# Optimization experiments

Hardware: AMD Instinct MI355X
Metric: run time of the kernel (lower is better)

## Reference

```python
import jax, jax.numpy as jnp
import numpy as np

B, T, D, H = 256, 512, 128, 256


def setup_inputs() -> dict:
    key = jax.random.key(0)
    ks = jax.random.split(key, 8)
    return {
        "x": jax.random.normal(ks[0], (B, T, D), jnp.float32),
        "m": jax.random.randint(ks[1], (B, T, D), 0, 2, jnp.int32),
        "s": jax.random.uniform(ks[2], (B, T, 1), jnp.float32),
        "kernel": jax.random.normal(ks[3], (D, 3 * H), jnp.float32) * 0.05,
        "recurrent_kernel": jax.random.normal(ks[4], (H, 3 * H), jnp.float32) * 0.05,
        "masking_kernel": jax.random.normal(ks[5], (D, 3 * H), jnp.float32) * 0.05,
        "bias": jnp.zeros((3 * H,), jnp.float32),
        "input_decay_kernel": jax.random.normal(ks[6], (D,), jnp.float32) * 0.05,
        "input_decay_bias": jnp.zeros((D,), jnp.float32),
        "hidden_decay_kernel": jax.random.normal(ks[7], (D, H), jnp.float32) * 0.05,
        "hidden_decay_bias": jnp.zeros((H,), jnp.float32),
    }


def _grud_scan(x, m, s, kernel, recurrent_kernel, masking_kernel, bias,
               input_decay_kernel, input_decay_bias,
               hidden_decay_kernel, hidden_decay_bias):
    b, t, d = x.shape
    h = recurrent_kernel.shape[0]
    mf = m.astype(x.dtype)
    mb = m > 0  # boolean mask, K.switch semantics
    # mask projection is h-independent -> hoist the big GEMM out of the scan
    mproj = jnp.einsum('btd,dk->btk', mf, masking_kernel)  # [B,T,3H]
    Kz, Kr, Kh = kernel[:, :h], kernel[:, h:2 * h], kernel[:, 2 * h:]
    Rz, Rr, Rh = recurrent_kernel[:, :h], recurrent_kernel[:, h:2 * h], recurrent_kernel[:, 2 * h:]
    bz, br, bh = bias[:h], bias[h:2 * h], bias[2 * h:]

    def step(carry, inp):
        h_tm1, x_keep, s_prev = carry
        xt, mbt, st, mpt = inp  # xt [B,D], mbt [B,D] bool, st [B,1], mpt [B,3H]
        d_t = st - s_prev  # [B,D] via broadcast
        gamma_di = jnp.exp(-jax.nn.relu(d_t * input_decay_kernel + input_decay_bias))
        gamma_dh = jnp.exp(-jax.nn.relu(d_t @ hidden_decay_kernel + hidden_decay_bias))
        x_keep_t = jnp.where(mbt, xt, x_keep)
        x_t = jnp.where(mbt, xt, gamma_di * x_keep_t)
        h_d = gamma_dh * h_tm1
        mz, mr, mh = mpt[:, :h], mpt[:, h:2 * h], mpt[:, 2 * h:]
        z_t = jax.nn.sigmoid(x_t @ Kz + h_d @ Rz + mz + bz)
        r_pre = x_t @ Kr + h_d @ Rr + mr + br  # original uses pre-activation r in hh
        hh_t = jnp.tanh(x_t @ Kh + (r_pre * h_d) @ Rh + mh + bh)
        h_t = z_t * h_tm1 + (1.0 - z_t) * hh_t
        s_keep = jnp.where(mbt, jnp.broadcast_to(st, s_prev.shape), s_prev)
        return (h_t, x_keep_t, s_keep), h_t

    init = (jnp.zeros((b, h), x.dtype), jnp.zeros((b, d), x.dtype), jnp.zeros((b, d), x.dtype))
    xs = (jnp.swapaxes(x, 0, 1), jnp.swapaxes(mb, 0, 1),
          jnp.swapaxes(s, 0, 1), jnp.swapaxes(mproj, 0, 1))
    _, hs = jax.lax.scan(step, init, xs)  # hs: [T,B,H]
    return jnp.swapaxes(hs, 0, 1)  # [B,T,H]


def reference(x, m, s, kernel, recurrent_kernel, masking_kernel, bias,
              input_decay_kernel, input_decay_bias,
              hidden_decay_kernel, hidden_decay_bias):
    return _grud_scan(x, m, s, kernel, recurrent_kernel, masking_kernel, bias,
                      input_decay_kernel, input_decay_bias,
                      hidden_decay_kernel, hidden_decay_bias)
```

## Files before the change

kernel.cpp:

```cpp
#include <hip/hip_runtime.h>
#include <hip/hip_bf16.h>
#include <cstdint>


#define Bsz 256
#define Tsz 512
#define Dsz 128
#define Hsz 256
#define BT  (Bsz * Tsz)
#define N3H 768

typedef __attribute__((ext_vector_type(8))) short   short8;
typedef __attribute__((ext_vector_type(8))) __bf16  bf16x8;
typedef __attribute__((ext_vector_type(4))) float   f32x4;

__device__ __forceinline__ unsigned short f2bf(float f) {
    union { float f; unsigned u; } v; v.f = f;
    unsigned r = v.u + 0x7fffu + ((v.u >> 16) & 1u);
    return (unsigned short)(r >> 16);
}
__device__ __forceinline__ float b2f(unsigned short u) {
    union { unsigned u; float f; } v; v.u = ((unsigned)u) << 16;
    return v.f;
}
__device__ __forceinline__ bf16x8 ld_frag(const unsigned short* p) {
    short8 v = *(const short8*)p;
    return __builtin_bit_cast(bf16x8, v);
}

__device__ __forceinline__ void barrier_lds() {
    asm volatile("s_waitcnt lgkmcnt(0)\n\ts_barrier" ::: "memory");
}

__global__ void k_pack(const float* __restrict__ kern, const float* __restrict__ maskk,
                       const float* __restrict__ rk,   const float* __restrict__ hdk,
                       unsigned short* __restrict__ KM_T, unsigned short* __restrict__ R_T,
                       unsigned short* __restrict__ W_T) {
    int i = blockIdx.x * 256 + threadIdx.x;
    if (i < N3H * 256) {
        int n = i >> 8, k = i & 255;
        float v = (k < 128) ? kern[k * N3H + n] : maskk[(k - 128) * N3H + n];
        KM_T[i] = f2bf(v);
        R_T[i]  = f2bf(rk[k * N3H + n]);
    } else {
        int j = i - N3H * 256;
        if (j < 256 * 128) {
            int n = j >> 7, k = j & 127;
            W_T[j] = f2bf(hdk[k * 256 + n]);
        }
    }
}

__global__ __launch_bounds__(256) void k_locf(
        const float* __restrict__ x, const int* __restrict__ m,
        const float* __restrict__ s, const float* __restrict__ wdi,
        const float* __restrict__ bdi,
        unsigned short* __restrict__ X2, unsigned short* __restrict__ Dt) {
    int gid = blockIdx.x * blockDim.x + threadIdx.x;
    int b = gid >> 7, d = gid & 127;
    float w  = wdi[d], bi = bdi[d];
    float x_keep = 0.f, s_prev = 0.f;
    const float* xb  = x + (size_t)b * Tsz * Dsz + d;
    const int*   mb_ = m + (size_t)b * Tsz * Dsz + d;
    const float* sb  = s + (size_t)b * Tsz;
    unsigned short* X2b = X2 + (size_t)b * Tsz * 256 + d;
    unsigned short* Dtb = Dt + (size_t)b * Tsz * 128 + d;
    for (int t0 = 0; t0 < Tsz; t0 += 4) {
        float xv[4], sv[4]; int mv[4];
#pragma unroll
        for (int u = 0; u < 4; u++) {
            xv[u] = xb[(size_t)(t0 + u) * Dsz];
            mv[u] = mb_[(size_t)(t0 + u) * Dsz];
            sv[u] = sb[t0 + u];
        }
#pragma unroll
        for (int u = 0; u < 4; u++) {
            int t = t0 + u;
            float dt  = sv[u] - s_prev;
            float gdi = __expf(-fmaxf(dt * w + bi, 0.f));
            bool  mbt = mv[u] > 0;
            if (mbt) x_keep = xv[u];
            float xe = mbt ? xv[u] : gdi * x_keep;
            if (mbt) s_prev = sv[u];
            X2b[(size_t)t * 256]       = f2bf(xe);
            X2b[(size_t)t * 256 + 128] = f2bf((float)mv[u]);
            Dtb[(size_t)t * 128]       = f2bf(dt);
        }
    }
}

template <int MODE, int K, int N>
__global__ __launch_bounds__(256) void k_gemm(
        const unsigned short* __restrict__ A, const unsigned short* __restrict__ Bt,
        const float* __restrict__ bias, unsigned short* __restrict__ C) {
    __shared__ unsigned short As[128][40];
    __shared__ unsigned short Bs[128][40];
    int m0 = blockIdx.x * 128, n0 = blockIdx.y * 128;
    int tid = threadIdx.x, lane = tid & 63, w = tid >> 6;
    int wm = w & 1, wn = w >> 1;
    int r15 = lane & 15, q = lane >> 4;
    int arow = tid >> 2, akg = tid & 3;
    f32x4 acc[4][4];
#pragma unroll
    for (int i = 0; i < 4; i++)
#pragma unroll
        for (int j = 0; j < 4; j++) acc[i][j] = f32x4{0.f, 0.f, 0.f, 0.f};

    for (int kk = 0; kk < K; kk += 32) {
        short8 av0 = *(const short8*)(A  + (size_t)(m0 + arow)      * K + kk + akg * 8);
        short8 av1 = *(const short8*)(A  + (size_t)(m0 + arow + 64) * K + kk + akg * 8);
        short8 bv0 = *(const short8*)(Bt + (size_t)(n0 + arow)      * K + kk + akg * 8);
        short8 bv1 = *(const short8*)(Bt + (size_t)(n0 + arow + 64) * K + kk + akg * 8);
        *(short8*)&As[arow][akg * 8]      = av0;
        *(short8*)&As[arow + 64][akg * 8] = av1;
        *(short8*)&Bs[arow][akg * 8]      = bv0;
        *(short8*)&Bs[arow + 64][akg * 8] = bv1;
        __syncthreads();
        bf16x8 af[4], bf[4];
#pragma unroll
        for (int i = 0; i < 4; i++) af[i] = ld_frag(&As[wm * 64 + i * 16 + r15][q * 8]);
#pragma unroll
        for (int j = 0; j < 4; j++) bf[j] = ld_frag(&Bs[wn * 64 + j * 16 + r15][q * 8]);
#pragma unroll
        for (int i = 0; i < 4; i++)
#pragma unroll
            for (int j = 0; j < 4; j++)
                acc[i][j] = __builtin_amdgcn_mfma_f32_16x16x32_bf16(af[i], bf[j], acc[i][j], 0, 0, 0);
        __syncthreads();
    }
#pragma unroll
    for (int i = 0; i < 4; i++)
#pragma unroll
        for (int j = 0; j < 4; j++) {
            int col = n0 + wn * 64 + j * 16 + r15;
            float bs = bias[col];
#pragma unroll
            for (int rg = 0; rg < 4; rg++) {
                int row = m0 + wm * 64 + i * 16 + q * 4 + rg;
                float v = acc[i][j][rg] + bs;
                if (MODE == 1) v = __expf(-fmaxf(v, 0.f));
                C[(size_t)row * N + col] = f2bf(v);
            }
        }
}

__global__ __launch_bounds__(512, 2) void k_scan(
        const unsigned short* __restrict__ Apre, const unsigned short* __restrict__ G,
        const unsigned short* __restrict__ R_T, float* __restrict__ out) {
    int b = blockIdx.x;
    int tid = threadIdx.x, lane = tid & 63, w = tid >> 6;
    int r15 = lane & 15, q = lane >> 4;

    __shared__ __align__(16) unsigned short hd_bf[256];
    __shared__ __align__(16) unsigned short u_bf[256];
    __shared__ __align__(16) unsigned short ap_l[2][768];
    __shared__ __align__(16) unsigned short g_l[2][256];

    bf16x8 fzr[4][8];
    bf16x8 fh[2][8];
#pragma unroll
    for (int nt = 0; nt < 4; nt++) {
        int col = (nt < 2) ? (w * 32 + nt * 16 + r15)
                           : (256 + w * 32 + (nt - 2) * 16 + r15);
        const unsigned short* base = R_T + (size_t)col * 256 + q * 8;
#pragma unroll
        for (int kt = 0; kt < 8; kt++) {
            fzr[nt][kt] = ld_frag(base + kt * 32);
            asm volatile("" : "+v"(fzr[nt][kt]));
        }
    }
#pragma unroll
    for (int nt = 0; nt < 2; nt++) {
        const unsigned short* base = R_T + (size_t)(512 + w * 32 + nt * 16 + r15) * 256 + q * 8;
#pragma unroll
        for (int kt = 0; kt < 8; kt++) {
            fh[nt][kt] = ld_frag(base + kt * 32);
            asm volatile("" : "+v"(fh[nt][kt]));
        }
    }

    if (tid < 256) hd_bf[tid] = 0;

    const unsigned short* aprow = Apre + (size_t)b * Tsz * N3H;
    const unsigned short* grow  = G    + (size_t)b * Tsz * 256;

    if (tid < 192)      *(uint2*)&ap_l[0][tid * 4]         = *(const uint2*)(aprow + tid * 4);
    else if (tid < 384) *(uint2*)&ap_l[1][(tid-192) * 4]   = *(const uint2*)(aprow + N3H + (tid-192) * 4);
    else if (tid < 448) *(uint2*)&g_l[0][(tid-384) * 4]    = *(const uint2*)(grow + (tid-384) * 4);
    else                *(uint2*)&g_l[1][(tid-448) * 4]    = *(const uint2*)(grow + 256 + (tid-448) * 4);
    __syncthreads();

    bool hiSel  = (q >= 2);
    bool writer = ((q & 1) == 0);
    int  col    = w * 32 + (hiSel ? 16 : 0) + r15;
    float h_reg  = 0.f;
    float hd_reg = 0.f;

    float* outb = out + (size_t)b * Tsz * 256;
    for (int t = 0; t < Tsz; t++) {
        int buf = t & 1;
        int tp2 = (t + 2 < Tsz) ? t + 2 : Tsz - 1;
        unsigned pf;
        if (tid < 384) pf = *(const unsigned*)(aprow + (size_t)tp2 * N3H + tid * 2);
        else           pf = *(const unsigned*)(grow  + (size_t)tp2 * 256 + (tid - 384) * 2);

        unsigned short a_z = ap_l[buf][col];
        unsigned short a_r = ap_l[buf][256 + col];
        unsigned short a_h = ap_l[buf][512 + col];

        f32x4 acc[4];
#pragma unroll
        for (int nt = 0; nt < 4; nt++) acc[nt] = f32x4{0.f, 0.f, 0.f, 0.f};
#pragma unroll
        for (int kt = 0; kt < 8; kt++) {
            bf16x8 afr = ld_frag(&hd_bf[kt * 32 + q * 8]);
#pragma unroll
            for (int nt = 0; nt < 4; nt++)
                acc[nt] = __builtin_amdgcn_mfma_f32_16x16x32_bf16(afr, fzr[nt][kt], acc[nt], 0, 0, 0);
        }
        float pz = (hiSel ? acc[1][0] : acc[0][0]) + b2f(a_z);
        float pr = (hiSel ? acc[3][0] : acc[2][0]) + b2f(a_r);
        float u  = pr * hd_reg;
        if (writer) u_bf[col] = f2bf(u);
        barrier_lds();

        unsigned short g_v = g_l[buf ^ 1][col];
        f32x4 acch[2];
#pragma unroll
        for (int nt = 0; nt < 2; nt++) acch[nt] = f32x4{0.f, 0.f, 0.f, 0.f};
#pragma unroll
        for (int kt = 0; kt < 8; kt++) {
            bf16x8 afr = ld_frag(&u_bf[kt * 32 + q * 8]);
#pragma unroll
            for (int nt = 0; nt < 2; nt++)
                acch[nt] = __builtin_amdgcn_mfma_f32_16x16x32_bf16(afr, fh[nt][kt], acch[nt], 0, 0, 0);
        }
        float z = 1.f / (1.f + __expf(-pz));
        float ph = (hiSel ? acch[1][0] : acch[0][0]) + b2f(a_h);
        float e2 = __expf(2.f * ph);
        float hh = 1.f - 2.f / (e2 + 1.f);
        float hn = z * h_reg + (1.f - z) * hh;
        h_reg = hn;
        if (writer) outb[(size_t)t * 256 + col] = hn;
        hd_reg = b2f(g_v) * hn;
        if (writer) hd_bf[col] = f2bf(hd_reg);
        barrier_lds();

        if (tid < 384) *(unsigned*)&ap_l[buf][tid * 2] = pf;
        else           *(unsigned*)&g_l[buf][(tid - 384) * 2] = pf;
    }
}

extern "C" void kernel_launch(void* const* d_in, const int* in_sizes, int n_in,
                              void* d_out, int out_size, void* d_ws, size_t ws_size,
                              hipStream_t stream) {
    const float* x    = (const float*)d_in[0];
    const int*   m    = (const int*)  d_in[1];
    const float* s    = (const float*)d_in[2];
    const float* kern = (const float*)d_in[3];
    const float* rk   = (const float*)d_in[4];
    const float* mk   = (const float*)d_in[5];
    const float* bias = (const float*)d_in[6];
    const float* wdi  = (const float*)d_in[7];
    const float* bdi  = (const float*)d_in[8];
    const float* hdk  = (const float*)d_in[9];
    const float* hdb  = (const float*)d_in[10];
    float* out = (float*)d_out;

    char* ws = (char*)d_ws;
    size_t off = 0;
    auto alloc = [&](size_t bytes) -> void* {
        void* p = ws + off; off += (bytes + 255) & ~(size_t)255; return p;
    };
    unsigned short* X2   = (unsigned short*)alloc((size_t)BT * 256 * 2);
    unsigned short* Dt   = (unsigned short*)alloc((size_t)BT * 128 * 2);
    unsigned short* Apre = (unsigned short*)alloc((size_t)BT * N3H * 2);
    unsigned short* Gm   = (unsigned short*)alloc((size_t)BT * 256 * 2);
    unsigned short* KM_T = (unsigned short*)alloc((size_t)N3H * 256 * 2);
    unsigned short* R_T  = (unsigned short*)alloc((size_t)N3H * 256 * 2);
    unsigned short* W_T  = (unsigned short*)alloc((size_t)256 * 128 * 2);
    (void)ws_size; (void)in_sizes; (void)n_in; (void)out_size;

    k_pack<<<dim3((N3H * 256 + 256 * 128 + 255) / 256), dim3(256), 0, stream>>>(
        kern, mk, rk, hdk, KM_T, R_T, W_T);
    k_locf<<<dim3(Bsz * Dsz / 256), dim3(256), 0, stream>>>(x, m, s, wdi, bdi, X2, Dt);
    k_gemm<0, 256, N3H><<<dim3(BT / 128, N3H / 128), dim3(256), 0, stream>>>(X2, KM_T, bias, Apre);
    k_gemm<1, 128, 256><<<dim3(BT / 128, 256 / 128), dim3(256), 0, stream>>>(Dt, W_T, hdb, Gm);
    k_scan<<<dim3(Bsz), dim3(512), 0, stream>>>(Apre, Gm, R_T, out);
}
```

Before: 1.066 ms.

## Load GEMM tiles straight into LDS with XOR swizzle and swap grid order

Result: no change. 1.071 ms (+0.4%).

```diff
diff --git a/kernel.cpp b/kernel.cpp
--- a/kernel.cpp
+++ b/kernel.cpp
@@ -13,6 +13,9 @@
 typedef __attribute__((ext_vector_type(8))) short   short8;
 typedef __attribute__((ext_vector_type(8))) __bf16  bf16x8;
 typedef __attribute__((ext_vector_type(4))) float   f32x4;
+
+typedef const __attribute__((address_space(1))) unsigned char gas_t;
+typedef __attribute__((address_space(3))) unsigned char las_t;
 
 __device__ __forceinline__ unsigned short f2bf(float f) {
     union { float f; unsigned u; } v; v.f = f;
@@ -93,13 +96,15 @@
 __global__ __launch_bounds__(256) void k_gemm(
         const unsigned short* __restrict__ A, const unsigned short* __restrict__ Bt,
         const float* __restrict__ bias, unsigned short* __restrict__ C) {
-    __shared__ unsigned short As[128][40];
-    __shared__ unsigned short Bs[128][40];
-    int m0 = blockIdx.x * 128, n0 = blockIdx.y * 128;
+    __shared__ unsigned short As[128 * 32];
+    __shared__ unsigned short Bs[128 * 32];
+    int n0 = blockIdx.x * 128, m0 = blockIdx.y * 128;
     int tid = threadIdx.x, lane = tid & 63, w = tid >> 6;
     int wm = w & 1, wn = w >> 1;
     int r15 = lane & 15, q = lane >> 4;
-    int arow = tid >> 2, akg = tid & 3;
+
+    int srow0 = w * 16 + (lane >> 2);
+    int chnkL = lane & 3;
     f32x4 acc[4][4];
 #pragma unroll
     for (int i = 0; i < 4; i++)
@@ -107,20 +112,29 @@
         for (int j = 0; j < 4; j++) acc[i][j] = f32x4{0.f, 0.f, 0.f, 0.f};
 
     for (int kk = 0; kk < K; kk += 32) {
-        short8 av0 = *(const short8*)(A  + (size_t)(m0 + arow)      * K + kk + akg * 8);
-        short8 av1 = *(const short8*)(A  + (size_t)(m0 + arow + 64) * K + kk + akg * 8);
-        short8 bv0 = *(const short8*)(Bt + (size_t)(n0 + arow)      * K + kk + akg * 8);
-        short8 bv1 = *(const short8*)(Bt + (size_t)(n0 + arow + 64) * K + kk + akg * 8);
-        *(short8*)&As[arow][akg * 8]      = av0;
-        *(short8*)&As[arow + 64][akg * 8] = av1;
-        *(short8*)&Bs[arow][akg * 8]      = bv0;
-        *(short8*)&Bs[arow + 64][akg * 8] = bv1;
+#pragma unroll
+        for (int j = 0; j < 2; j++) {
+            int row = srow0 + j * 64;
+            int csrc = chnkL ^ (row & 3);
+            const unsigned short* ga = A  + (size_t)(m0 + row) * K + kk + csrc * 8;
+            const unsigned short* gb = Bt + (size_t)(n0 + row) * K + kk + csrc * 8;
+            las_t* la = (las_t*)As + (size_t)(j * 4096 + w * 1024 + (lane & 63) * 16);
+            las_t* lb = (las_t*)Bs + (size_t)(j * 4096 + w * 1024 + (lane & 63) * 16);
+            __builtin_amdgcn_global_load_lds((gas_t*)ga, la, 16, 0, 0);
+            __builtin_amdgcn_global_load_lds((gas_t*)gb, lb, 16, 0, 0);
+        }
         __syncthreads();
         bf16x8 af[4], bf[4];
 #pragma unroll
-        for (int i = 0; i < 4; i++) af[i] = ld_frag(&As[wm * 64 + i * 16 + r15][q * 8]);
-#pragma unroll
-        for (int j = 0; j < 4; j++) bf[j] = ld_frag(&Bs[wn * 64 + j * 16 + r15][q * 8]);
+        for (int i = 0; i < 4; i++) {
+            int row = wm * 64 + i * 16 + r15;
+            af[i] = ld_frag(&As[row * 32 + ((q ^ (row & 3)) << 3)]);
+        }
+#pragma unroll
+        for (int j = 0; j < 4; j++) {
+            int row = wn * 64 + j * 16 + r15;
+            bf[j] = ld_frag(&Bs[row * 32 + ((q ^ (row & 3)) << 3)]);
+        }
 #pragma unroll
         for (int i = 0; i < 4; i++)
 #pragma unroll
@@ -226,14 +240,13 @@
 
         unsigned short g_v = g_l[buf ^ 1][col];
         f32x4 acch[2];
-#pragma unroll
-        for (int nt = 0; nt < 2; nt++) acch[nt] = f32x4{0.f, 0.f, 0.f, 0.f};
+        acch[0] = f32x4{0.f, 0.f, 0.f, 0.f};
+        acch[1] = f32x4{0.f, 0.f, 0.f, 0.f};
 #pragma unroll
         for (int kt = 0; kt < 8; kt++) {
             bf16x8 afr = ld_frag(&u_bf[kt * 32 + q * 8]);
-#pragma unroll
-            for (int nt = 0; nt < 2; nt++)
-                acch[nt] = __builtin_amdgcn_mfma_f32_16x16x32_bf16(afr, fh[nt][kt], acch[nt], 0, 0, 0);
+            acch[0] = __builtin_amdgcn_mfma_f32_16x16x32_bf16(afr, fh[0][kt], acch[0], 0, 0, 0);
+            acch[1] = __builtin_amdgcn_mfma_f32_16x16x32_bf16(afr, fh[1][kt], acch[1], 0, 0, 0);
         }
         float z = 1.f / (1.f + __expf(-pz));
         float ph = (hiSel ? acch[1][0] : acch[0][0]) + b2f(a_h);
@@ -284,7 +297,7 @@
     k_pack<<<dim3((N3H * 256 + 256 * 128 + 255) / 256), dim3(256), 0, stream>>>(
         kern, mk, rk, hdk, KM_T, R_T, W_T);
     k_locf<<<dim3(Bsz * Dsz / 256), dim3(256), 0, stream>>>(x, m, s, wdi, bdi, X2, Dt);
-    k_gemm<0, 256, N3H><<<dim3(BT / 128, N3H / 128), dim3(256), 0, stream>>>(X2, KM_T, bias, Apre);
-    k_gemm<1, 128, 256><<<dim3(BT / 128, 256 / 128), dim3(256), 0, stream>>>(Dt, W_T, hdb, Gm);
+    k_gemm<0, 256, N3H><<<dim3(N3H / 128, BT / 128), dim3(256), 0, stream>>>(X2, KM_T, bias, Apre);
+    k_gemm<1, 128, 256><<<dim3(256 / 128, BT / 128), dim3(256), 0, stream>>>(Dt, W_T, hdb, Gm);
     k_scan<<<dim3(Bsz), dim3(512), 0, stream>>>(Apre, Gm, R_T, out);
 }
```
